# Optimization experiments

Measured on AMD Instinct MI355X. Metric: run time of the kernel, lower is better.

Reference implementation:

```python
import jax, jax.numpy as jnp
import numpy as np

B_SZ, SEQ, D_MODEL, D_INNER, D_STATE, D_CONV = 2, 2048, 768, 1536, 16, 4
EPS = 1e-6


def setup_inputs() -> dict:
    key = jax.random.key(0)
    ks = jax.random.split(key, 8)
    sc = lambda n: 1.0 / np.sqrt(n)
    x = jax.random.normal(ks[0], (B_SZ, SEQ, D_MODEL), jnp.float32)
    norm_w = jnp.ones((D_MODEL,), jnp.float32)
    w_in = jax.random.normal(ks[1], (D_MODEL, 2 * D_INNER), jnp.float32) * sc(D_MODEL)
    conv_w = jax.random.normal(ks[2], (D_INNER, D_CONV), jnp.float32) * sc(D_CONV)
    conv_b = jnp.zeros((D_INNER,), jnp.float32)
    w_x = jax.random.normal(ks[3], (D_INNER, 2 * D_STATE + 1), jnp.float32) * sc(D_INNER)
    w_dt = jax.random.normal(ks[4], (D_INNER,), jnp.float32)
    b_dt = jnp.zeros((D_INNER,), jnp.float32)
    A_log = jnp.log(jnp.broadcast_to(jnp.arange(1, D_STATE + 1, dtype=jnp.float32), (D_INNER, D_STATE)))
    D = jnp.ones((D_INNER,), jnp.float32)
    w_out = jax.random.normal(ks[5], (D_INNER, D_MODEL), jnp.float32) * sc(D_INNER)
    return dict(x=x, norm_w=norm_w, w_in=w_in, conv_w=conv_w, conv_b=conv_b,
                w_x=w_x, w_dt=w_dt, b_dt=b_dt, A_log=A_log, D=D, w_out=w_out)


def _rmsnorm(x, w):
    xf = x.astype(jnp.float32)
    rms = jax.lax.rsqrt(jnp.mean(xf * xf, axis=-1, keepdims=True) + EPS)
    return (xf * rms).astype(x.dtype) * w


def _silu(x):
    return x * jax.nn.sigmoid(x)


def _s6_forward(x, norm_w, w_in, conv_w, conv_b, w_x, w_dt, b_dt, A_log, D, w_out):
    Bsz, S, Dm = x.shape
    Di, K = conv_w.shape
    Ds = A_log.shape[1]
    residual = x
    xn = _rmsnorm(x, norm_w)
    xz = xn @ w_in                                 # (B,S,2*Di)
    x_main, z = jnp.split(xz, 2, axis=-1)
    # causal depthwise conv1d: pad left K-1, keep first S outputs
    lhs = x_main.transpose(0, 2, 1)                # (B,Di,S)
    rhs = conv_w[:, None, :]                       # (Di,1,K)
    conv = jax.lax.conv_general_dilated(
        lhs, rhs, window_strides=(1,), padding=[(K - 1, 0)],
        dimension_numbers=('NCH', 'OIH', 'NCH'), feature_group_count=Di)
    x_main = (conv + conv_b[None, :, None]).transpose(0, 2, 1)  # (B,S,Di)
    x_main = _silu(x_main)
    x_ssm = x_main @ w_x                           # (B,S,2*Ds+1)
    Bp = x_ssm[..., :Ds]                           # (B,S,Ds)
    Cp = x_ssm[..., Ds:2 * Ds]                     # (B,S,Ds)
    dt_raw = x_ssm[..., -1:]                       # (B,S,1)
    dt = jax.nn.softplus(dt_raw * w_dt[None, None, :] + b_dt)  # (B,S,Di)
    A = -jnp.exp(A_log)                            # (Di,Ds)

    def step(h, inp):
        xt, dtt, Bt, Ct = inp                      # (B,Di),(B,Di),(B,Ds),(B,Ds)
        dA = jnp.exp(A[None] * dtt[..., None])     # (B,Di,Ds)
        h = dA * h + (dtt * xt)[..., None] * Bt[:, None, :]
        y = jnp.einsum('bds,bs->bd', h, Ct)
        return h, y

    h0 = jnp.zeros((Bsz, Di, Ds), x_main.dtype)
    xs = (x_main.transpose(1, 0, 2), dt.transpose(1, 0, 2),
          Bp.transpose(1, 0, 2), Cp.transpose(1, 0, 2))
    _, ys = jax.lax.scan(step, h0, xs)             # ys: (S,B,Di)
    y = ys.transpose(1, 0, 2)
    y = y + x_main * D
    y = y * _silu(z)
    return residual + y @ w_out                    # dropout is identity at eval


def reference(x, norm_w, w_in, conv_w, conv_b, w_x, w_dt, b_dt, A_log, D, w_out):
    return _s6_forward(x, norm_w, w_in, conv_w, conv_b, w_x, w_dt, b_dt, A_log, D, w_out)
```

## Files before the change

kernel.cpp:

```cpp
#include <hip/hip_runtime.h>
#include <math.h>


#define DM   768
#define DI   1536
#define DS2  16
#define SEQN 2048
#define BSZ  2
#define NROWS (BSZ*SEQN)
#define CHUNK 32
#define NCHUNK (SEQN/CHUNK)

#define AS1 __attribute__((address_space(1)))
#define AS3 __attribute__((address_space(3)))

typedef short short8 __attribute__((ext_vector_type(8)));
typedef short short4v __attribute__((ext_vector_type(4)));
typedef float f32x4 __attribute__((ext_vector_type(4)));

__device__ __forceinline__ unsigned short f2bf(float f) {
  unsigned u = __builtin_bit_cast(unsigned, f);
  unsigned r = (u + 0x7FFFu + ((u >> 16) & 1u)) >> 16;
  return (unsigned short)r;
}
__device__ __forceinline__ float bf2f(short s) {
  unsigned u = ((unsigned)(unsigned short)s) << 16;
  return __builtin_bit_cast(float, u);
}

template<int N> __device__ __forceinline__ void waitcnt_vm() {
  if constexpr (N == 0)      asm volatile("s_waitcnt vmcnt(0)" ::: "memory");
  else if constexpr (N == 2) asm volatile("s_waitcnt vmcnt(2)" ::: "memory");
  else if constexpr (N == 3) asm volatile("s_waitcnt vmcnt(3)" ::: "memory");
  else if constexpr (N == 4) asm volatile("s_waitcnt vmcnt(4)" ::: "memory");
  else if constexpr (N == 6) asm volatile("s_waitcnt vmcnt(6)" ::: "memory");
  else if constexpr (N == 8) asm volatile("s_waitcnt vmcnt(8)" ::: "memory");
}

__device__ __forceinline__ void transpose_body(const float* __restrict__ src,
                                               int rows, int cols,
                                               short* __restrict__ dst,
                                               int bx, int by, int tid) {
  __shared__ float t[32][33];
  int r0 = by * 32, c0 = bx * 32;
  int lr = tid >> 3, lc4 = (tid & 7) * 4;
  float4 v = *reinterpret_cast<const float4*>(&src[(size_t)(r0 + lr) * cols + c0 + lc4]);
  t[lr][lc4 + 0] = v.x; t[lr][lc4 + 1] = v.y; t[lr][lc4 + 2] = v.z; t[lr][lc4 + 3] = v.w;
  __syncthreads();
  int orow = tid >> 3, oc4 = (tid & 7) * 4;
  short4v o;
  o.x = (short)f2bf(t[oc4 + 0][orow]); o.y = (short)f2bf(t[oc4 + 1][orow]);
  o.z = (short)f2bf(t[oc4 + 2][orow]); o.w = (short)f2bf(t[oc4 + 3][orow]);
  *reinterpret_cast<short4v*>(&dst[(size_t)(c0 + orow) * rows + r0 + oc4]) = o;
}

__global__ __launch_bounds__(256) void prep_k(
    const float* __restrict__ x, const float* __restrict__ nw,
    short* __restrict__ xn,
    const float* __restrict__ w_in, short* __restrict__ winT,
    const float* __restrict__ w_out, short* __restrict__ woutT,
    const float* __restrict__ wx, float* __restrict__ wxT) {
  const int bid = blockIdx.x;
  const int tid = threadIdx.x;
  if (bid < 1024) {
    int wv = tid >> 6, lane = tid & 63;
    int row = bid * 4 + wv;
    const float* xr = x + (size_t)row * DM;
    float4 v[3];
    float s = 0.f;
#pragma unroll
    for (int i = 0; i < 3; ++i) {
      v[i] = *reinterpret_cast<const float4*>(&xr[(i * 64 + lane) * 4]);
      s = fmaf(v[i].x, v[i].x, s); s = fmaf(v[i].y, v[i].y, s);
      s = fmaf(v[i].z, v[i].z, s); s = fmaf(v[i].w, v[i].w, s);
    }
#pragma unroll
    for (int off = 32; off >= 1; off >>= 1) s += __shfl_xor(s, off, 64);
    float rs = rsqrtf(s * (1.f / DM) + 1e-6f);
#pragma unroll
    for (int i = 0; i < 3; ++i) {
      const float4 w = *reinterpret_cast<const float4*>(&nw[(i * 64 + lane) * 4]);
      short4v o;
      o.x = (short)f2bf(v[i].x * rs * w.x); o.y = (short)f2bf(v[i].y * rs * w.y);
      o.z = (short)f2bf(v[i].z * rs * w.z); o.w = (short)f2bf(v[i].w * rs * w.w);
      *reinterpret_cast<short4v*>(&xn[(size_t)row * DM + (i * 64 + lane) * 4]) = o;
    }
  } else if (bid < 1024 + 2304) {
    int i2 = bid - 1024;
    transpose_body(w_in, DM, 2 * DI, winT, i2 % 96, i2 / 96, tid);
  } else if (bid < 1024 + 2304 + 1152) {
    int i3 = bid - (1024 + 2304);
    transpose_body(w_out, DI, DM, woutT, i3 % 24, i3 / 24, tid);
  } else {
    int idx = (bid - (1024 + 2304 + 1152)) * 256 + tid;
    if (idx < DI * 33) {
      int k = idx / 33, j = idx % 33;
      wxT[(size_t)j * DI + k] = wx[idx];
    }
  }
}

template<int BM, int BN, bool OUTBF>
__global__ __launch_bounds__(512) void gemm_bf16(
    const short* __restrict__ A, int lda,
    const short* __restrict__ Bt, int ldb,
    void* __restrict__ Cv, int ldc, int K,
    const float* __restrict__ res, int ldr)
{
  constexpr int WM = BM / 2, WN = BN / 4;
  constexpr int MI = WM / 16, NJ = WN / 16;
  constexpr int ACH = BM / 8, BCH = BN / 8;
  constexpr int CPW = (ACH + BCH) / 8;
  static_assert((ACH + BCH) % 8 == 0, "chunks must split across 8 waves");
  __shared__ __align__(16) short As[2 * BM * 64];
  __shared__ __align__(16) short Bs[2 * BN * 64];
  const int tid = threadIdx.x;
  const int w = tid >> 6, lane = tid & 63;
  const int wr = w >> 2, wc = w & 3;
  const int m0 = blockIdx.y * BM, n0 = blockIdx.x * BN;
  const int l15 = lane & 15, l4 = lane >> 4;
  const int srow = lane >> 3;
  const int ksw = (((lane & 7) ^ srow) * 8);
  const int rx = l15 & 7;

  f32x4 acc[MI][NJ];
#pragma unroll
  for (int i = 0; i < MI; ++i)
#pragma unroll
    for (int j = 0; j < NJ; ++j) acc[i][j] = (f32x4){0.f, 0.f, 0.f, 0.f};

  auto STAGE = [&](int buf, int k0) {
#pragma unroll
    for (int q = 0; q < CPW; ++q) {
      int c = w * CPW + q;
      if (c < ACH) {
        __builtin_amdgcn_global_load_lds(
            (const AS1 unsigned int*)(A + (size_t)(m0 + 8 * c + srow) * lda + k0 + ksw),
            (AS3 unsigned int*)((char*)As + buf * (BM * 128) + c * 1024), 16, 0, 0);
      } else {
        int c2 = c - ACH;
        __builtin_amdgcn_global_load_lds(
            (const AS1 unsigned int*)(Bt + (size_t)(n0 + 8 * c2 + srow) * ldb + k0 + ksw),
            (AS3 unsigned int*)((char*)Bs + buf * (BN * 128) + c2 * 1024), 16, 0, 0);
      }
    }
  };

  STAGE(0, 0);
  int cur = 0;
  const int NT = K / 64;
  for (int t = 0; t < NT; ++t) {
    __builtin_amdgcn_sched_barrier(0);
    __builtin_amdgcn_s_barrier();
    if (t + 1 < NT) {
      STAGE(cur ^ 1, (t + 1) * 64);
      waitcnt_vm<CPW>();
    } else {
      waitcnt_vm<0>();
    }
    __builtin_amdgcn_sched_barrier(0);
    __builtin_amdgcn_s_barrier();
    __builtin_amdgcn_sched_barrier(0);
    const short* Ab = As + cur * BM * 64;
    const short* Bb = Bs + cur * BN * 64;
    __builtin_amdgcn_s_setprio(1);
#pragma unroll
    for (int kk = 0; kk < 2; ++kk) {
      short8 a[MI], b[NJ];
#pragma unroll
      for (int i = 0; i < MI; ++i)
        a[i] = *reinterpret_cast<const short8*>(
            &Ab[(wr * WM + i * 16 + l15) * 64 + (((kk * 4 + l4) ^ rx) * 8)]);
#pragma unroll
      for (int j = 0; j < NJ; ++j)
        b[j] = *reinterpret_cast<const short8*>(
            &Bb[(wc * WN + j * 16 + l15) * 64 + (((kk * 4 + l4) ^ rx) * 8)]);
#pragma unroll
      for (int i = 0; i < MI; ++i)
#pragma unroll
        for (int j = 0; j < NJ; ++j)
          acc[i][j] = __builtin_amdgcn_mfma_f32_16x16x32_bf16(a[i], b[j], acc[i][j], 0, 0, 0);
    }
    __builtin_amdgcn_s_setprio(0);
    cur ^= 1;
  }

#pragma unroll
  for (int i = 0; i < MI; ++i) {
#pragma unroll
    for (int j = 0; j < NJ; ++j) {
      int col = n0 + wc * WN + j * 16 + l15;
#pragma unroll
      for (int r = 0; r < 4; ++r) {
        int row = m0 + wr * WM + i * 16 + l4 * 4 + r;
        float v = acc[i][j][r];
        if constexpr (OUTBF) {
          ((short*)Cv)[(size_t)row * ldc + col] = (short)f2bf(v);
        } else {
          if (res) v += res[(size_t)row * ldr + col];
          ((float*)Cv)[(size_t)row * ldc + col] = v;
        }
      }
    }
  }
}

__global__ __launch_bounds__(256) void conv_xssm_k(
    const short* __restrict__ xz,
    const float* __restrict__ cw, const float* __restrict__ cb,
    const float* __restrict__ wxT,
    short* __restrict__ xc,
    float* __restrict__ Bm, float* __restrict__ Cm, float* __restrict__ dtr)
{
  const int wv = threadIdx.x >> 6, lane = threadIdx.x & 63;
  const int r0 = blockIdx.x * 8 + wv * 2;
  const int t0 = r0 & (SEQN - 1);
  float a0[33], a1[33];
#pragma unroll
  for (int j = 0; j < 33; ++j) { a0[j] = 0.f; a1[j] = 0.f; }

  for (int it = 0; it < 6; ++it) {
    const int k0 = lane * 4 + it * 256;
    short4v rb[5];
#pragma unroll
    for (int rr = 0; rr < 5; ++rr) {
      int trow = t0 - 3 + rr;
      if (trow >= 0)
        rb[rr] = *reinterpret_cast<const short4v*>(&xz[(size_t)(r0 - 3 + rr) * 3072 + k0]);
      else
        rb[rr] = (short4v){0, 0, 0, 0};
    }
    const float4 bias = *reinterpret_cast<const float4*>(&cb[k0]);
    float x0v[4], x1v[4];
    short4v o0, o1;
#pragma unroll
    for (int i = 0; i < 4; ++i) {
      const float4 cwv = *reinterpret_cast<const float4*>(&cw[(size_t)(k0 + i) * 4]);
      const float bi = (i == 0) ? bias.x : (i == 1) ? bias.y : (i == 2) ? bias.z : bias.w;
      float acc0 = bi, acc1 = bi;
      acc0 = fmaf(bf2f(rb[0][i]), cwv.x, acc0);
      acc0 = fmaf(bf2f(rb[1][i]), cwv.y, acc0);
      acc0 = fmaf(bf2f(rb[2][i]), cwv.z, acc0);
      acc0 = fmaf(bf2f(rb[3][i]), cwv.w, acc0);
      acc1 = fmaf(bf2f(rb[1][i]), cwv.x, acc1);
      acc1 = fmaf(bf2f(rb[2][i]), cwv.y, acc1);
      acc1 = fmaf(bf2f(rb[3][i]), cwv.z, acc1);
      acc1 = fmaf(bf2f(rb[4][i]), cwv.w, acc1);
      float s0 = acc0 / (1.f + __expf(-acc0));
      float s1 = acc1 / (1.f + __expf(-acc1));
      short u0 = (short)f2bf(s0), u1 = (short)f2bf(s1);
      o0[i] = u0; o1[i] = u1;
      x0v[i] = bf2f(u0); x1v[i] = bf2f(u1);
    }
    *reinterpret_cast<short4v*>(&xc[(size_t)r0 * DI + k0]) = o0;
    *reinterpret_cast<short4v*>(&xc[(size_t)(r0 + 1) * DI + k0]) = o1;
#pragma unroll
    for (int j = 0; j < 33; ++j) {
      const float4 wq = *reinterpret_cast<const float4*>(&wxT[(size_t)j * DI + k0]);
      a0[j] = fmaf(x0v[0], wq.x, fmaf(x0v[1], wq.y, fmaf(x0v[2], wq.z, fmaf(x0v[3], wq.w, a0[j]))));
      a1[j] = fmaf(x1v[0], wq.x, fmaf(x1v[1], wq.y, fmaf(x1v[2], wq.z, fmaf(x1v[3], wq.w, a1[j]))));
    }
  }
#pragma unroll
  for (int j = 0; j < 33; ++j) {
#pragma unroll
    for (int off = 32; off >= 1; off >>= 1) {
      a0[j] += __shfl_xor(a0[j], off, 64);
      a1[j] += __shfl_xor(a1[j], off, 64);
    }
  }
  if (lane == 0) {
#pragma unroll
    for (int j = 0; j < 16; ++j) Bm[(size_t)r0 * 16 + j] = a0[j];
#pragma unroll
    for (int j = 0; j < 16; ++j) Cm[(size_t)r0 * 16 + j] = a0[16 + j];
    dtr[r0] = a0[32];
#pragma unroll
    for (int j = 0; j < 16; ++j) Bm[(size_t)(r0 + 1) * 16 + j] = a1[j];
#pragma unroll
    for (int j = 0; j < 16; ++j) Cm[(size_t)(r0 + 1) * 16 + j] = a1[16 + j];
    dtr[r0 + 1] = a1[32];
  }
}

__global__ __launch_bounds__(256) void scan_part1(
    const short* __restrict__ xc,
    const float* __restrict__ Bm, const float* __restrict__ dtr,
    const float* __restrict__ w_dt, const float* __restrict__ b_dt,
    const float* __restrict__ A_log,
    float* __restrict__ hL, float* __restrict__ Tsum)
{
  const int blk = blockIdx.x;
  const int c  = blk % NCHUNK;
  const int db = (blk / NCHUNK) % (DI / 256);
  const int b  = blk / (NCHUNK * (DI / 256));
  const int tid = threadIdx.x;
  const int d = db * 256 + tid;
  const size_t cb = (size_t)b * SEQN + c * CHUNK;

  __shared__ float sB[CHUNK][16];
  __shared__ float sdt[CHUNK];
  if (tid < CHUNK * 4)
    reinterpret_cast<float4*>(&sB[0][0])[tid] =
        reinterpret_cast<const float4*>(&Bm[cb * 16])[tid];
  if (tid < CHUNK / 4)
    reinterpret_cast<float4*>(sdt)[tid] =
        reinterpret_cast<const float4*>(&dtr[cb])[tid];
  __syncthreads();

  const float wdt = w_dt[d], bdt = b_dt[d];
  float a[DS2], h[DS2];
#pragma unroll
  for (int q = 0; q < 4; ++q) {
    float4 al = *reinterpret_cast<const float4*>(&A_log[(size_t)d * DS2 + q * 4]);
    a[q * 4 + 0] = -__expf(al.x); a[q * 4 + 1] = -__expf(al.y);
    a[q * 4 + 2] = -__expf(al.z); a[q * 4 + 3] = -__expf(al.w);
  }
#pragma unroll
  for (int n = 0; n < DS2; ++n) h[n] = 0.f;
  float T = 0.f;

#pragma unroll 2
  for (int tt = 0; tt < CHUNK; ++tt) {
    float v = fmaf(sdt[tt], wdt, bdt);
    float dtv = (v > 15.f) ? v : __logf(1.f + __expf(v));
    T += dtv;
    float xv = bf2f(xc[(cb + tt) * DI + d]);
    float s = dtv * xv;
    float bb[DS2];
#pragma unroll
    for (int q = 0; q < 4; ++q)
      *reinterpret_cast<float4*>(&bb[q * 4]) =
          *reinterpret_cast<const float4*>(&sB[tt][q * 4]);
#pragma unroll
    for (int n = 0; n < DS2; ++n)
      h[n] = fmaf(__expf(a[n] * dtv), h[n], s * bb[n]);
  }

  const size_t base = (size_t)(b * NCHUNK + c) * DI + d;
#pragma unroll
  for (int q = 0; q < 4; ++q)
    *reinterpret_cast<float4*>(&hL[base * 16 + q * 4]) =
        *reinterpret_cast<const float4*>(&h[q * 4]);
  Tsum[base] = T;
}

__global__ __launch_bounds__(256) void scan_combine_k(
    float* __restrict__ hLH, const float* __restrict__ Tsum,
    const float* __restrict__ A_log)
{
  int g = blockIdx.x * 256 + threadIdx.x;
  int n = g & 15;
  int d = (g >> 4) % DI;
  int b = g / (DI * DS2);
  const float a = -__expf(A_log[(size_t)d * DS2 + n]);
  float h = 0.f;
  for (int c = 0; c < NCHUNK; ++c) {
    size_t base = (size_t)(b * NCHUNK + c) * DI + d;
    float hl = hLH[base * 16 + n];
    float T = Tsum[base];
    float hprev = h;
    h = fmaf(__expf(a * T), h, hl);
    hLH[base * 16 + n] = hprev;
  }
}

__global__ __launch_bounds__(256) void scan_part3(
    const short* __restrict__ xc,
    const short* __restrict__ xz,
    short* __restrict__ ybf,
    const float* __restrict__ Bm, const float* __restrict__ Cm,
    const float* __restrict__ dtr,
    const float* __restrict__ w_dt, const float* __restrict__ b_dt,
    const float* __restrict__ A_log, const float* __restrict__ Dp,
    const float* __restrict__ Hinit)
{
  const int blk = blockIdx.x;
  const int c  = blk % NCHUNK;
  const int db = (blk / NCHUNK) % (DI / 256);
  const int b  = blk / (NCHUNK * (DI / 256));
  const int tid = threadIdx.x;
  const int d = db * 256 + tid;
  const size_t cb = (size_t)b * SEQN + c * CHUNK;

  __shared__ float sB[CHUNK][16], sC[CHUNK][16];
  __shared__ float sdt[CHUNK];
  if (tid < CHUNK * 4)
    reinterpret_cast<float4*>(&sB[0][0])[tid] =
        reinterpret_cast<const float4*>(&Bm[cb * 16])[tid];
  else if (tid < CHUNK * 8)
    reinterpret_cast<float4*>(&sC[0][0])[tid - CHUNK * 4] =
        reinterpret_cast<const float4*>(&Cm[cb * 16])[tid - CHUNK * 4];
  if (tid < CHUNK / 4)
    reinterpret_cast<float4*>(sdt)[tid] =
        reinterpret_cast<const float4*>(&dtr[cb])[tid];

  const float wdt = w_dt[d], bdt = b_dt[d];
  const float Dd = Dp[d];
  float a[DS2], h[DS2];
#pragma unroll
  for (int q = 0; q < 4; ++q) {
    float4 al = *reinterpret_cast<const float4*>(&A_log[(size_t)d * DS2 + q * 4]);
    a[q * 4 + 0] = -__expf(al.x); a[q * 4 + 1] = -__expf(al.y);
    a[q * 4 + 2] = -__expf(al.z); a[q * 4 + 3] = -__expf(al.w);
  }
  const size_t base = (size_t)(b * NCHUNK + c) * DI + d;
#pragma unroll
  for (int q = 0; q < 4; ++q)
    *reinterpret_cast<float4*>(&h[q * 4]) =
        *reinterpret_cast<const float4*>(&Hinit[base * 16 + q * 4]);
  __syncthreads();

#pragma unroll 2
  for (int tt = 0; tt < CHUNK; ++tt) {
    float v = fmaf(sdt[tt], wdt, bdt);
    float dtv = (v > 15.f) ? v : __logf(1.f + __expf(v));
    float xv = bf2f(xc[(cb + tt) * DI + d]);
    float s = dtv * xv;
    float bb[DS2], cc[DS2];
#pragma unroll
    for (int q = 0; q < 4; ++q) {
      *reinterpret_cast<float4*>(&bb[q * 4]) =
          *reinterpret_cast<const float4*>(&sB[tt][q * 4]);
      *reinterpret_cast<float4*>(&cc[q * 4]) =
          *reinterpret_cast<const float4*>(&sC[tt][q * 4]);
    }
    float y = 0.f;
#pragma unroll
    for (int n = 0; n < DS2; ++n) {
      h[n] = fmaf(__expf(a[n] * dtv), h[n], s * bb[n]);
      y = fmaf(h[n], cc[n], y);
    }
    const size_t rr = cb + tt;
    float z = bf2f(xz[rr * 3072 + DI + d]);
    float yo = fmaf(xv, Dd, y);
    ybf[rr * DI + d] = (short)f2bf(yo * (z / (1.f + __expf(-z))));
  }
}

extern "C" void kernel_launch(void* const* d_in, const int* in_sizes, int n_in,
                              void* d_out, int out_size, void* d_ws, size_t ws_size,
                              hipStream_t stream) {
  const float* x      = (const float*)d_in[0];
  const float* norm_w = (const float*)d_in[1];
  const float* w_in   = (const float*)d_in[2];
  const float* conv_w = (const float*)d_in[3];
  const float* conv_b = (const float*)d_in[4];
  const float* w_x    = (const float*)d_in[5];
  const float* w_dt   = (const float*)d_in[6];
  const float* b_dt   = (const float*)d_in[7];
  const float* A_log  = (const float*)d_in[8];
  const float* Dp     = (const float*)d_in[9];
  const float* w_out  = (const float*)d_in[10];
  float* out = (float*)d_out;

  float* ws   = (float*)d_ws;
  float* Bm   = ws;
  float* Cm   = Bm + (size_t)NROWS * 16;
  float* dtr  = Cm + (size_t)NROWS * 16;
  float* hL   = dtr + NROWS;
  float* Tsum = hL + (size_t)BSZ * NCHUNK * DI * 16;
  float* wxT  = Tsum + (size_t)BSZ * NCHUNK * DI;
  short* xzb  = (short*)(wxT + (size_t)33 * DI);
  short* xcb  = xzb + (size_t)NROWS * 2 * DI;
  short* xnb  = xcb + (size_t)NROWS * DI;
  short* winT = xnb + (size_t)NROWS * DM;
  short* woutT= winT + (size_t)2 * DI * DM;
  short* ybf  = woutT + (size_t)DM * DI;

  prep_k<<<1024 + 2304 + 1152 + 198, 256, 0, stream>>>(
      x, norm_w, xnb, w_in, winT, w_out, woutT, w_x, wxT);

  gemm_bf16<128, 128, true><<<dim3(2 * DI / 128, NROWS / 128), 512, 0, stream>>>(
      xnb, DM, winT, DM, xzb, 2 * DI, DM, nullptr, 0);

  conv_xssm_k<<<NROWS / 8, 256, 0, stream>>>(xzb, conv_w, conv_b, wxT,
                                             xcb, Bm, Cm, dtr);

  const int nblk = BSZ * (DI / 256) * NCHUNK;
  scan_part1<<<nblk, 256, 0, stream>>>(xcb, Bm, dtr, w_dt, b_dt, A_log, hL, Tsum);
  scan_combine_k<<<(BSZ * DI * DS2) / 256, 256, 0, stream>>>(hL, Tsum, A_log);
  scan_part3<<<nblk, 256, 0, stream>>>(xcb, xzb, ybf, Bm, Cm, dtr, w_dt, b_dt,
                                       A_log, Dp, hL);

  gemm_bf16<128, 64, false><<<dim3(DM / 64, NROWS / 128), 512, 0, stream>>>(
      ybf, DI, woutT, DI, out, DM, DI, x, DM);
}
```

Before: 157.3 us.

## Stage w_x projection weights through double-buffered LDS in conv_xssm kernel

The conv+SiLU phase now runs first, keeping each lane's bf16 outputs in registers. The x_ssm projection then runs in a second phase that reads wxT from a shared, double-buffered LDS tile filled with async global_load_lds. The four waves each load 9 of 36 padded rows, so a block fetches the weights once instead of once per wave. In exchange it adds barriers and waitcnt-based pipelining, uses 72 KB of LDS per block (which can limit occupancy), and pads the wxT workspace to 36 rows.

```diff
diff --git a/kernel.cpp b/kernel.cpp
--- a/kernel.cpp
+++ b/kernel.cpp
@@ -35,6 +35,7 @@
   else if constexpr (N == 4) asm volatile("s_waitcnt vmcnt(4)" ::: "memory");
   else if constexpr (N == 6) asm volatile("s_waitcnt vmcnt(6)" ::: "memory");
   else if constexpr (N == 8) asm volatile("s_waitcnt vmcnt(8)" ::: "memory");
+  else if constexpr (N == 9) asm volatile("s_waitcnt vmcnt(9)" ::: "memory");
 }
 
 __device__ __forceinline__ void transpose_body(const float* __restrict__ src,
@@ -212,26 +213,25 @@
     short* __restrict__ xc,
     float* __restrict__ Bm, float* __restrict__ Cm, float* __restrict__ dtr)
 {
-  const int wv = threadIdx.x >> 6, lane = threadIdx.x & 63;
+  __shared__ __align__(16) float wxs[2][36][256];
+  const int tid = threadIdx.x;
+  const int wv = tid >> 6, lane = tid & 63;
   const int r0 = blockIdx.x * 8 + wv * 2;
   const int t0 = r0 & (SEQN - 1);
-  float a0[33], a1[33];
-#pragma unroll
-  for (int j = 0; j < 33; ++j) { a0[j] = 0.f; a1[j] = 0.f; }
-
+
+  short4v xs0[6], xs1[6];
+#pragma unroll
   for (int it = 0; it < 6; ++it) {
     const int k0 = lane * 4 + it * 256;
     short4v rb[5];
 #pragma unroll
     for (int rr = 0; rr < 5; ++rr) {
       int trow = t0 - 3 + rr;
-      if (trow >= 0)
-        rb[rr] = *reinterpret_cast<const short4v*>(&xz[(size_t)(r0 - 3 + rr) * 3072 + k0]);
-      else
-        rb[rr] = (short4v){0, 0, 0, 0};
+      rb[rr] = (trow >= 0)
+          ? *reinterpret_cast<const short4v*>(&xz[(size_t)(r0 - 3 + rr) * 3072 + k0])
+          : (short4v){0, 0, 0, 0};
     }
     const float4 bias = *reinterpret_cast<const float4*>(&cb[k0]);
-    float x0v[4], x1v[4];
     short4v o0, o1;
 #pragma unroll
     for (int i = 0; i < 4; ++i) {
@@ -248,19 +248,53 @@
       acc1 = fmaf(bf2f(rb[4][i]), cwv.w, acc1);
       float s0 = acc0 / (1.f + __expf(-acc0));
       float s1 = acc1 / (1.f + __expf(-acc1));
-      short u0 = (short)f2bf(s0), u1 = (short)f2bf(s1);
-      o0[i] = u0; o1[i] = u1;
-      x0v[i] = bf2f(u0); x1v[i] = bf2f(u1);
+      o0[i] = (short)f2bf(s0); o1[i] = (short)f2bf(s1);
     }
     *reinterpret_cast<short4v*>(&xc[(size_t)r0 * DI + k0]) = o0;
     *reinterpret_cast<short4v*>(&xc[(size_t)(r0 + 1) * DI + k0]) = o1;
+    xs0[it] = o0; xs1[it] = o1;
+  }
+
+  float a0[33], a1[33];
+#pragma unroll
+  for (int j = 0; j < 33; ++j) { a0[j] = 0.f; a1[j] = 0.f; }
+
+  auto STAGE = [&](int buf, int c) {
+#pragma unroll
+    for (int q = 0; q < 9; ++q) {
+      int j = wv * 9 + q;
+      __builtin_amdgcn_global_load_lds(
+          (const AS1 unsigned int*)(wxT + (size_t)j * DI + c * 256 + lane * 4),
+          (AS3 unsigned int*)(&wxs[buf][j][0]), 16, 0, 0);
+    }
+  };
+
+  STAGE(0, 0);
+#pragma unroll
+  for (int c = 0; c < 6; ++c) {
+    const int cur = c & 1;
+    __builtin_amdgcn_sched_barrier(0);
+    __builtin_amdgcn_s_barrier();
+    if (c + 1 < 6) {
+      STAGE(cur ^ 1, c + 1);
+      waitcnt_vm<9>();
+    } else {
+      waitcnt_vm<0>();
+    }
+    __builtin_amdgcn_sched_barrier(0);
+    __builtin_amdgcn_s_barrier();
+    __builtin_amdgcn_sched_barrier(0);
+    float x0v[4], x1v[4];
+#pragma unroll
+    for (int i = 0; i < 4; ++i) { x0v[i] = bf2f(xs0[c][i]); x1v[i] = bf2f(xs1[c][i]); }
 #pragma unroll
     for (int j = 0; j < 33; ++j) {
-      const float4 wq = *reinterpret_cast<const float4*>(&wxT[(size_t)j * DI + k0]);
+      const float4 wq = *reinterpret_cast<const float4*>(&wxs[cur][j][lane * 4]);
       a0[j] = fmaf(x0v[0], wq.x, fmaf(x0v[1], wq.y, fmaf(x0v[2], wq.z, fmaf(x0v[3], wq.w, a0[j]))));
       a1[j] = fmaf(x1v[0], wq.x, fmaf(x1v[1], wq.y, fmaf(x1v[2], wq.z, fmaf(x1v[3], wq.w, a1[j]))));
     }
   }
+
 #pragma unroll
   for (int j = 0; j < 33; ++j) {
 #pragma unroll
@@ -461,7 +495,7 @@
   float* hL   = dtr + NROWS;
   float* Tsum = hL + (size_t)BSZ * NCHUNK * DI * 16;
   float* wxT  = Tsum + (size_t)BSZ * NCHUNK * DI;
-  short* xzb  = (short*)(wxT + (size_t)33 * DI);
+  short* xzb  = (short*)(wxT + (size_t)36 * DI);
   short* xcb  = xzb + (size_t)NROWS * 2 * DI;
   short* xnb  = xcb + (size_t)NROWS * DI;
   short* winT = xnb + (size_t)NROWS * DM;
```

New measurement: 165.2 us. +5.0%, slower.
